# Performance work log

Hardware: AMD Instinct MI355X
Metric: run time of the kernel (lower is better)

The kernel has to match this reference:

```python
import jax, jax.numpy as jnp
import numpy as np

B, N, M, D = 128, 4096, 64, 16
SQRT_D = 4
SCALE = 1.0 / (D ** 0.5)
LN_EPS = 1e-5


def setup_inputs() -> dict:
    key = jax.random.key(0)
    k1, k2, k3 = jax.random.split(key, 3)
    w_const = np.sqrt(M / (SQRT_D * N)).astype(np.float32)
    return {
        "input": jax.random.normal(k1, (B, N, D), dtype=jnp.float32),
        "next_capsule_value": jax.random.normal(k2, (B, M, D), dtype=jnp.float32),
        "w": w_const * jax.random.normal(k3, (N, SQRT_D, SQRT_D, M), dtype=jnp.float32),
        "ln_w": jnp.ones((D,), dtype=jnp.float32),
        "ln_b": jnp.zeros((D,), dtype=jnp.float32),
        "num_iter": 1,
    }


def reference(input, next_capsule_value, w, ln_w, ln_b, num_iter):
    b = input.shape[0]
    # matrix-pose view: [B, N, sqrt_d, sqrt_d] and [B, M, sqrt_d, sqrt_d]
    x = input.reshape(b, N, SQRT_D, SQRT_D)
    ncv = next_capsule_value.reshape(b, M, SQRT_D, SQRT_D)
    # QK-like routing scores: [B, N, M]
    qk = jnp.einsum('bnax,nxdm,bmad->bnm', x, w, ncv) * SCALE
    qk = jax.nn.softmax(qk, axis=2)
    qk = qk / (jnp.sum(qk, axis=2, keepdims=True) + 1e-10)
    # weighted aggregation -> [B, M, sqrt_d, sqrt_d] -> [B, M, D]
    out = jnp.einsum('bnm,bnax,nxdm->bmad', qk, x, w).reshape(b, M, D)
    # dropout rate = 0.0 -> identity; LayerNorm over last dim
    mu = jnp.mean(out, axis=-1, keepdims=True)
    var = jnp.var(out, axis=-1, keepdims=True)
    out = (out - mu) * jax.lax.rsqrt(var + LN_EPS) * ln_w + ln_b
    return out
```

## Files before the change

kernel.cpp:

```cpp
#include <hip/hip_runtime.h>
#include <stdint.h>

#define B_ 128
#define N_ 4096
#define M_ 64
#define D_ 16
#define NSLICE 128
#define SLICE_N 32
#define OUT_ELEMS (B_ * M_ * D_)
#define OUT4 (OUT_ELEMS / 4)

#if __has_builtin(__builtin_amdgcn_exp2f)
#define EXP2F(x) __builtin_amdgcn_exp2f(x)
#else
#define EXP2F(x) __expf((x) * 0.69314718f)
#endif

template<int CTRL, int RM, int BC>
__device__ __forceinline__ float dpp_f(float old, float src) {
  return __int_as_float(__builtin_amdgcn_update_dpp(
      __float_as_int(old), __float_as_int(src), CTRL, RM, 0xF, BC));
}

__device__ __forceinline__ float wave_sum64(float x) {
  x += dpp_f<0x121, 0xF, 1>(0.f, x);
  x += dpp_f<0x122, 0xF, 1>(0.f, x);
  x += dpp_f<0x124, 0xF, 1>(0.f, x);
  x += dpp_f<0x128, 0xF, 1>(0.f, x);
  x += dpp_f<0x142, 0xA, 1>(0.f, x);
  x += dpp_f<0x143, 0xC, 1>(0.f, x);
  return __int_as_float(__builtin_amdgcn_readlane(__float_as_int(x), 63));
}

template<int EPI>
__global__ __launch_bounds__(256, 4)
void capsule_main(const float* __restrict__ x_in, const float* __restrict__ ncv_in,
                  const float* __restrict__ w_in, float* __restrict__ dst) {
  const int L     = blockIdx.x;
  const int bg    = L >> 7;
  const int inner = L & 127;
  const int s     = ((inner & 7) << 4) | (inner >> 3);
  const int lane  = threadIdx.x & 63;
  const int wid   = __builtin_amdgcn_readfirstlane((int)(threadIdx.x >> 6));
  const int t     = threadIdx.x;
  const int b0    = bg * 8 + wid * 2;
  const int n0    = s * SLICE_N;

  __shared__ float xls[8 * SLICE_N * D_];

#pragma unroll
  for (int k = 0; k < 4; ++k) {
    const int g   = t + 256 * k;
    const int b8  = g >> 7;
    const int rem = g & 127;
    ((float4*)xls)[g] =
        ((const float4*)x_in)[((size_t)(bg * 8 + b8) * N_ + n0) * 4 + rem];
  }

  const float QS = 0.25f * 1.44269504f;
  float ncv[2][16];
#pragma unroll
  for (int bb = 0; bb < 2; ++bb) {
    const float4* p = (const float4*)(ncv_in + ((size_t)(b0 + bb) * M_ + lane) * D_);
#pragma unroll
    for (int q = 0; q < 4; ++q) {
      float4 v = p[q];
      ncv[bb][q*4+0] = v.x * QS; ncv[bb][q*4+1] = v.y * QS;
      ncv[bb][q*4+2] = v.z * QS; ncv[bb][q*4+3] = v.w * QS;
    }
  }

  float acc[2][16];
#pragma unroll
  for (int bb = 0; bb < 2; ++bb)
#pragma unroll
    for (int j = 0; j < 16; ++j) acc[bb][j] = 0.f;

  __syncthreads();

  const float* wp = w_in + (size_t)n0 * 1024 + lane;

#pragma unroll 2
  for (int i = 0; i < SLICE_N; ++i) {
    float wv[16];
#pragma unroll
    for (int xd = 0; xd < 16; ++xd) wv[xd] = wp[(size_t)i * 1024 + xd * 64];

#pragma unroll
    for (int bb = 0; bb < 2; ++bb) {
      const float4* xp4 = (const float4*)&xls[((wid * 2 + bb) * SLICE_N + i) * D_];
      float xv[16];
#pragma unroll
      for (int q = 0; q < 4; ++q) {
        float4 v = xp4[q];
        xv[q*4+0] = v.x; xv[q*4+1] = v.y; xv[q*4+2] = v.z; xv[q*4+3] = v.w;
      }
      float vote[16];
#pragma unroll
      for (int a = 0; a < 4; ++a) {
#pragma unroll
        for (int d = 0; d < 4; ++d) {
          float v = xv[a*4+0] * wv[0*4+d];
          v = fmaf(xv[a*4+1], wv[1*4+d], v);
          v = fmaf(xv[a*4+2], wv[2*4+d], v);
          v = fmaf(xv[a*4+3], wv[3*4+d], v);
          vote[a*4+d] = v;
        }
      }
      float q0 = 0.f, q1 = 0.f, q2 = 0.f, q3 = 0.f;
#pragma unroll
      for (int j = 0; j < 4; ++j) {
        q0 = fmaf(vote[j],      ncv[bb][j],      q0);
        q1 = fmaf(vote[4 + j],  ncv[bb][4 + j],  q1);
        q2 = fmaf(vote[8 + j],  ncv[bb][8 + j],  q2);
        q3 = fmaf(vote[12 + j], ncv[bb][12 + j], q3);
      }
      const float sc = (q0 + q1) + (q2 + q3);
      const float p  = EXP2F(sc);
      const float sm = wave_sum64(p);
      const float rr = p * __builtin_amdgcn_rcpf(sm);
#pragma unroll
      for (int j = 0; j < 16; ++j) acc[bb][j] = fmaf(rr, vote[j], acc[bb][j]);
    }
  }

  if (EPI == 1) {
#pragma unroll
    for (int bb = 0; bb < 2; ++bb) {
      float4* op = (float4*)(dst + ((size_t)(s * B_ + b0 + bb) * M_ + lane) * D_);
#pragma unroll
      for (int q = 0; q < 4; ++q) {
        float4 v;
        v.x = acc[bb][q*4+0]; v.y = acc[bb][q*4+1];
        v.z = acc[bb][q*4+2]; v.w = acc[bb][q*4+3];
        op[q] = v;
      }
    }
  } else {
#pragma unroll
    for (int bb = 0; bb < 2; ++bb) {
      float* op = dst + ((size_t)(b0 + bb) * M_ + lane) * D_;
#pragma unroll
      for (int j = 0; j < 16; ++j) atomicAdd(op + j, acc[bb][j]);
    }
  }
}

__global__ void reduce_part(float4* __restrict__ ws4) {
  const int blk = blockIdx.x;
  const int sg  = blk >> 7;
  const int f   = ((blk & 127) << 8) + threadIdx.x;
  const size_t base = (size_t)(sg * 32) * OUT4 + f;
  float4 s0 = ws4[base];
  float4 s1 = ws4[base + OUT4];
#pragma unroll 4
  for (int k = 2; k < 32; k += 2) {
    float4 a = ws4[base + (size_t)k * OUT4];
    float4 b = ws4[base + (size_t)(k + 1) * OUT4];
    s0.x += a.x; s0.y += a.y; s0.z += a.z; s0.w += a.w;
    s1.x += b.x; s1.y += b.y; s1.z += b.z; s1.w += b.w;
  }
  float4 r;
  r.x = s0.x + s1.x; r.y = s0.y + s1.y; r.z = s0.z + s1.z; r.w = s0.w + s1.w;
  ws4[base] = r;
}

__global__ void reduce_ln2(const float4* __restrict__ ws4, float4* __restrict__ out4,
                           const float* __restrict__ lw, const float* __restrict__ lb) {
  const int f = blockIdx.x * 256 + threadIdx.x;
  float4 s = ws4[f];
#pragma unroll
  for (int sg = 1; sg < 4; ++sg) {
    float4 a = ws4[(size_t)(sg * 32) * OUT4 + f];
    s.x += a.x; s.y += a.y; s.z += a.z; s.w += a.w;
  }
  float sv = (s.x + s.y) + (s.z + s.w);
  sv += __shfl_xor(sv, 1, 4);
  sv += __shfl_xor(sv, 2, 4);
  const float mu = sv * 0.0625f;
  float4 d;
  d.x = s.x - mu; d.y = s.y - mu; d.z = s.z - mu; d.w = s.w - mu;
  float s2 = (d.x*d.x + d.y*d.y) + (d.z*d.z + d.w*d.w);
  s2 += __shfl_xor(s2, 1, 4);
  s2 += __shfl_xor(s2, 2, 4);
  const float inv = rsqrtf(s2 * 0.0625f + 1e-5f);
  const float4 w4 = ((const float4*)lw)[f & 3];
  const float4 b4 = ((const float4*)lb)[f & 3];
  float4 o;
  o.x = d.x * inv * w4.x + b4.x; o.y = d.y * inv * w4.y + b4.y;
  o.z = d.z * inv * w4.z + b4.z; o.w = d.w * inv * w4.w + b4.w;
  out4[f] = o;
}

__global__ void capsule_ln(float* __restrict__ out, const float* __restrict__ lw,
                           const float* __restrict__ lb) {
  const int t = blockIdx.x * 256 + threadIdx.x;
  const float v = out[t];
  float sv = v;
#pragma unroll
  for (int m = 1; m < 16; m <<= 1) sv += __shfl_xor(sv, m, 16);
  const float mu = sv * 0.0625f;
  const float dv = v - mu;
  float s2 = dv * dv;
#pragma unroll
  for (int m = 1; m < 16; m <<= 1) s2 += __shfl_xor(s2, m, 16);
  out[t] = dv * rsqrtf(s2 * 0.0625f + 1e-5f) * lw[t & 15] + lb[t & 15];
}

extern "C" void kernel_launch(void* const* d_in, const int* in_sizes, int n_in,
                              void* d_out, int out_size, void* d_ws, size_t ws_size,
                              hipStream_t stream) {
  (void)in_sizes; (void)n_in; (void)out_size;
  const float* x_in = (const float*)d_in[0];
  const float* ncv  = (const float*)d_in[1];
  const float* w    = (const float*)d_in[2];
  const float* lw   = (const float*)d_in[3];
  const float* lb   = (const float*)d_in[4];
  float* out = (float*)d_out;

  const size_t need = (size_t)NSLICE * OUT_ELEMS * sizeof(float);
  if (ws_size >= need) {
    float* ws = (float*)d_ws;
    capsule_main<1><<<2048, 256, 0, stream>>>(x_in, ncv, w, ws);
    reduce_part<<<512, 256, 0, stream>>>((float4*)ws);
    reduce_ln2<<<OUT4 / 256, 256, 0, stream>>>((const float4*)ws, (float4*)out, lw, lb);
  } else {
    hipMemsetAsync(out, 0, sizeof(float) * OUT_ELEMS, stream);
    capsule_main<0><<<2048, 256, 0, stream>>>(x_in, ncv, w, out);
    capsule_ln<<<OUT_ELEMS / 256, 256, 0, stream>>>(out, lw, lb);
  }
}
```

Measured before the change: 197.9 us.

## Fuse slice reduction and LayerNorm into main kernel via per-group arrival counters

Each batch group's last four arriving blocks, detected with an agent-scope atomic counter, wait until all 128 slices have written their partials. They then reduce the partials and apply LayerNorm directly, which removes the two follow-up reduction kernels and their launches. The inner loop also gains explicit double buffering of the w loads, fetching the next row's weights while the current one is computed. In exchange it adds a memset of the counters, spin-waiting blocks, and a serial 128-deep reduction done by only four blocks per group.

```diff
diff --git a/kernel.cpp b/kernel.cpp
--- a/kernel.cpp
+++ b/kernel.cpp
@@ -7,8 +7,10 @@
 #define D_ 16
 #define NSLICE 128
 #define SLICE_N 32
+#define NBG 16
 #define OUT_ELEMS (B_ * M_ * D_)
 #define OUT4 (OUT_ELEMS / 4)
+#define PART_BYTES ((size_t)NSLICE * OUT_ELEMS * sizeof(float))
 
 #if __has_builtin(__builtin_amdgcn_exp2f)
 #define EXP2F(x) __builtin_amdgcn_exp2f(x)
@@ -35,7 +37,9 @@
 template<int EPI>
 __global__ __launch_bounds__(256, 4)
 void capsule_main(const float* __restrict__ x_in, const float* __restrict__ ncv_in,
-                  const float* __restrict__ w_in, float* __restrict__ dst) {
+                  const float* __restrict__ w_in, float* __restrict__ dst,
+                  float* __restrict__ out_final, const float* __restrict__ lw,
+                  const float* __restrict__ lb, int* __restrict__ cnt) {
   const int L     = blockIdx.x;
   const int bg    = L >> 7;
   const int inner = L & 127;
@@ -47,6 +51,7 @@
   const int n0    = s * SLICE_N;
 
   __shared__ float xls[8 * SLICE_N * D_];
+  __shared__ int   sh_role;
 
 #pragma unroll
   for (int k = 0; k < 4; ++k) {
@@ -78,14 +83,9 @@
 
   __syncthreads();
 
-  const float* wp = w_in + (size_t)n0 * 1024 + lane;
-
-#pragma unroll 2
-  for (int i = 0; i < SLICE_N; ++i) {
-    float wv[16];
-#pragma unroll
-    for (int xd = 0; xd < 16; ++xd) wv[xd] = wp[(size_t)i * 1024 + xd * 64];
-
+  const float* wpb = w_in + (size_t)n0 * 1024 + lane;
+
+  auto body = [&](int i, const float (&wv)[16]) {
 #pragma unroll
     for (int bb = 0; bb < 2; ++bb) {
       const float4* xp4 = (const float4*)&xls[((wid * 2 + bb) * SLICE_N + i) * D_];
@@ -122,28 +122,102 @@
 #pragma unroll
       for (int j = 0; j < 16; ++j) acc[bb][j] = fmaf(rr, vote[j], acc[bb][j]);
     }
-  }
-
-  if (EPI == 1) {
-#pragma unroll
-    for (int bb = 0; bb < 2; ++bb) {
-      float4* op = (float4*)(dst + ((size_t)(s * B_ + b0 + bb) * M_ + lane) * D_);
-#pragma unroll
-      for (int q = 0; q < 4; ++q) {
-        float4 v;
-        v.x = acc[bb][q*4+0]; v.y = acc[bb][q*4+1];
-        v.z = acc[bb][q*4+2]; v.w = acc[bb][q*4+3];
-        op[q] = v;
-      }
-    }
-  } else {
+  };
+
+  float wv0[16], wv1[16];
+#pragma unroll
+  for (int xd = 0; xd < 16; ++xd) wv0[xd] = wpb[xd * 64];
+#pragma unroll 1
+  for (int ii = 0; ii < SLICE_N / 2; ++ii) {
+    const int iA = 2 * ii, iB = 2 * ii + 1;
+    {
+      const float* p = wpb + (size_t)iB * 1024;
+#pragma unroll
+      for (int xd = 0; xd < 16; ++xd) wv1[xd] = p[xd * 64];
+    }
+    body(iA, wv0);
+    {
+      const int inx = (iA + 2) & (SLICE_N - 1);
+      const float* p = wpb + (size_t)inx * 1024;
+#pragma unroll
+      for (int xd = 0; xd < 16; ++xd) wv0[xd] = p[xd * 64];
+    }
+    body(iB, wv1);
+  }
+
+  if (EPI == 0) {
 #pragma unroll
     for (int bb = 0; bb < 2; ++bb) {
       float* op = dst + ((size_t)(b0 + bb) * M_ + lane) * D_;
 #pragma unroll
       for (int j = 0; j < 16; ++j) atomicAdd(op + j, acc[bb][j]);
     }
-  }
+    return;
+  }
+
+#pragma unroll
+  for (int bb = 0; bb < 2; ++bb) {
+    float4* op = (float4*)(dst + ((size_t)(s * B_ + b0 + bb) * M_ + lane) * D_);
+#pragma unroll
+    for (int q = 0; q < 4; ++q) {
+      float4 v;
+      v.x = acc[bb][q*4+0]; v.y = acc[bb][q*4+1];
+      v.z = acc[bb][q*4+2]; v.w = acc[bb][q*4+3];
+      op[q] = v;
+    }
+  }
+  if (EPI == 2) return;
+
+  __syncthreads();
+  if (t == 0) {
+    __threadfence();
+    const int old = __hip_atomic_fetch_add(&cnt[bg], 1, __ATOMIC_ACQ_REL,
+                                           __HIP_MEMORY_SCOPE_AGENT);
+    sh_role = old - (NSLICE - 4);
+  }
+  __syncthreads();
+  const int role = sh_role;
+  if (role < 0) return;
+  if (t == 0) {
+    while (__hip_atomic_load(&cnt[bg], __ATOMIC_ACQUIRE,
+                             __HIP_MEMORY_SCOPE_AGENT) < NSLICE)
+      __builtin_amdgcn_s_sleep(32);
+  }
+  __syncthreads();
+  __threadfence();
+
+  const float4* p4 = (const float4*)dst;
+  const size_t base = (size_t)bg * 2048 + role * 512 + t;
+  float4 a0 = {0.f, 0.f, 0.f, 0.f}, a1 = {0.f, 0.f, 0.f, 0.f};
+#pragma unroll 4
+  for (int sl = 0; sl < NSLICE; ++sl) {
+    const float4 u = p4[(size_t)sl * OUT4 + base];
+    const float4 v = p4[(size_t)sl * OUT4 + base + 256];
+    a0.x += u.x; a0.y += u.y; a0.z += u.z; a0.w += u.w;
+    a1.x += v.x; a1.y += v.y; a1.z += v.z; a1.w += v.w;
+  }
+  const float4 w4 = ((const float4*)lw)[t & 3];
+  const float4 b4 = ((const float4*)lb)[t & 3];
+  float4 o[2]; const float4 aa[2] = {a0, a1};
+#pragma unroll
+  for (int k = 0; k < 2; ++k) {
+    float4 sv4 = aa[k];
+    float sv = (sv4.x + sv4.y) + (sv4.z + sv4.w);
+    sv += __shfl_xor(sv, 1, 4);
+    sv += __shfl_xor(sv, 2, 4);
+    const float mu = sv * 0.0625f;
+    float4 d;
+    d.x = sv4.x - mu; d.y = sv4.y - mu; d.z = sv4.z - mu; d.w = sv4.w - mu;
+    float s2 = (d.x*d.x + d.y*d.y) + (d.z*d.z + d.w*d.w);
+    s2 += __shfl_xor(s2, 1, 4);
+    s2 += __shfl_xor(s2, 2, 4);
+    const float inv = rsqrtf(s2 * 0.0625f + 1e-5f);
+    o[k].x = d.x * inv * w4.x + b4.x; o[k].y = d.y * inv * w4.y + b4.y;
+    o[k].z = d.z * inv * w4.z + b4.z; o[k].w = d.w * inv * w4.w + b4.w;
+  }
+  float4* out4 = (float4*)out_final;
+  out4[base]       = o[0];
+  out4[base + 256] = o[1];
 }
 
 __global__ void reduce_part(float4* __restrict__ ws4) {
@@ -218,15 +292,19 @@
   const float* lb   = (const float*)d_in[4];
   float* out = (float*)d_out;
 
-  const size_t need = (size_t)NSLICE * OUT_ELEMS * sizeof(float);
-  if (ws_size >= need) {
+  if (ws_size >= PART_BYTES + 4096) {
     float* ws = (float*)d_ws;
-    capsule_main<1><<<2048, 256, 0, stream>>>(x_in, ncv, w, ws);
+    int* cnt = (int*)((char*)d_ws + PART_BYTES);
+    hipMemsetAsync(cnt, 0, NBG * sizeof(int), stream);
+    capsule_main<1><<<2048, 256, 0, stream>>>(x_in, ncv, w, ws, out, lw, lb, cnt);
+  } else if (ws_size >= PART_BYTES) {
+    float* ws = (float*)d_ws;
+    capsule_main<2><<<2048, 256, 0, stream>>>(x_in, ncv, w, ws, out, lw, lb, nullptr);
     reduce_part<<<512, 256, 0, stream>>>((float4*)ws);
     reduce_ln2<<<OUT4 / 256, 256, 0, stream>>>((const float4*)ws, (float4*)out, lw, lb);
   } else {
     hipMemsetAsync(out, 0, sizeof(float) * OUT_ELEMS, stream);
-    capsule_main<0><<<2048, 256, 0, stream>>>(x_in, ncv, w, out);
+    capsule_main<0><<<2048, 256, 0, stream>>>(x_in, ncv, w, out, out, lw, lb, nullptr);
     capsule_ln<<<OUT_ELEMS / 256, 256, 0, stream>>>(out, lw, lb);
   }
 }
```

Result: slower. 558.8 us (+182.4%).
